# Kernel tuning notes

Measured on AMD Instinct MI355X. Metric: run time of the kernel, lower is better.

## Reference

```python
import jax, jax.numpy as jnp
import numpy as np

B, N, C = 4, 2048, 1024
H, D = 16, 64  # num_heads, head_dim; C = H*D
R = 16         # lora rank
SCALE = D ** -0.5


def setup_inputs() -> dict:
    key = jax.random.key(0)
    ks = jax.random.split(key, 6)
    return {
        "query": jax.random.normal(ks[0], (B, N, C), dtype=jnp.float32),
        "mask": jax.random.normal(ks[1], (B, 1, N, N), dtype=jnp.float32),
        "W_qkv": jax.random.normal(ks[2], (C, 3 * C), dtype=jnp.float32) * (C ** -0.5),
        "magnitude": jnp.ones((1, H, 1, 1), dtype=jnp.float32),
        "W_loraA": jax.random.normal(ks[3], (C, R), dtype=jnp.float32) * (C ** -0.5),
        "W_loraB": jax.random.normal(ks[4], (R, C), dtype=jnp.float32) * (R ** -0.5),
        "W_proj": jax.random.normal(ks[5], (C, C), dtype=jnp.float32) * (C ** -0.5),
    }


def reference(query, mask, W_qkv, magnitude, W_loraA, W_loraB, W_proj):
    # qkv projection: [B,N,3C] -> [3,B,H,N,D]
    qkv = (query @ W_qkv).reshape(B, N, 3, H, D).transpose(2, 0, 3, 1, 4)
    q, k, v = qkv[0], qkv[1], qkv[2]
    # LoRA/DoRA delta fused into q before attention
    delta = (query @ W_loraA) @ W_loraB                     # [B,N,C]
    delta = delta.reshape(B, N, H, D).transpose(0, 2, 1, 3)  # [B,H,N,D]
    q = q + magnitude * delta
    # attention
    attn = jnp.einsum('bhnd,bhmd->bhnm', q, k) * SCALE + mask
    attn = jax.nn.softmax(attn, axis=-1)
    out = jnp.einsum('bhnm,bhmd->bhnd', attn, v)            # [B,H,N,D]
    out = out.transpose(0, 2, 1, 3).reshape(B, N, C)
    return out @ W_proj
```

## Files before the change

kernel.cpp:

```cpp
#include <hip/hip_runtime.h>
#include <hip/hip_bf16.h>

#define Bd 4
#define Nd 2048
#define Cd 1024
#define Hd 16
#define Dd 64
#define Rd 16
#define KAUG 1056
#define SCALEf 0.125f
#define PIT 72

using short8 = __attribute__((ext_vector_type(8))) short;
using f32x4  = __attribute__((ext_vector_type(4))) float;

static __device__ __forceinline__ ushort f2bf(float f) {
    __hip_bfloat16 h = __float2bfloat16(f);
    return *reinterpret_cast<ushort*>(&h);
}

#define GLOAD_LDS16(g, l) __builtin_amdgcn_global_load_lds( \
    (const __attribute__((address_space(1))) void*)(g),      \
    (__attribute__((address_space(3))) void*)(l), 16, 0, 0)

__global__ __launch_bounds__(256) void pack_a_kernel(
    const float* __restrict__ query, ushort* __restrict__ Aaug)
{
    const int row = blockIdx.x;
    const int t = threadIdx.x;
    const float4 v = *(const float4*)&query[(size_t)row * Cd + t * 4];
    ushort4 u;
    u.x = f2bf(v.x); u.y = f2bf(v.y); u.z = f2bf(v.z); u.w = f2bf(v.w);
    *(ushort4*)&Aaug[(size_t)row * KAUG + t * 4] = u;
}

__global__ __launch_bounds__(256) void pack_wat_kernel(
    const float* __restrict__ WA, ushort* __restrict__ WAT)
{
    const int idx = blockIdx.x * 256 + threadIdx.x;
    const int c = idx >> 4, r = idx & 15;
    WAT[r * 1024 + c] = f2bf(WA[idx]);
}

__global__ __launch_bounds__(64) void lora_mfma_kernel(
    const ushort* __restrict__ Aro, const ushort* __restrict__ WAT,
    ushort* __restrict__ Awr)
{
    const int lane = threadIdx.x;
    const int quad = lane >> 4, lc = lane & 15;
    const int row0 = blockIdx.x * 16;
    f32x4 acc = {0.f, 0.f, 0.f, 0.f};
    #pragma unroll 4
    for (int k0 = 0; k0 < 1024; k0 += 32) {
        const short8 a = *(const short8*)&Aro[(size_t)(row0 + lc) * KAUG + k0 + quad * 8];
        const short8 b = *(const short8*)&WAT[lc * 1024 + k0 + quad * 8];
        acc = __builtin_amdgcn_mfma_f32_16x16x32_bf16(a, b, acc, 0, 0, 0);
    }
    #pragma unroll
    for (int ri = 0; ri < 4; ++ri) {
        const size_t row = row0 + quad * 4 + ri;
        Awr[row * KAUG + 1024 + lc] = f2bf(acc[ri]);
        Awr[row * KAUG + 1040 + lc] = 0;
    }
}

__global__ __launch_bounds__(256) void pack_bqkv_kernel(
    const float* __restrict__ Wqkv, const float* __restrict__ WloraB,
    const float* __restrict__ magnitude, ushort* __restrict__ BT)
{
    __shared__ float tile[32][33];
    const int k0 = blockIdx.x * 32, n0 = blockIdx.y * 32;
    const int tx = threadIdx.x & 31, ty = threadIdx.x >> 5;
    #pragma unroll
    for (int i = 0; i < 4; ++i) {
        const int k = k0 + ty + i * 8;
        const int n = n0 + tx;
        float v;
        if (k < 1024)                      v = Wqkv[(size_t)k * 3072 + n];
        else if (k < 1040 && n < 1024)     v = magnitude[n >> 6] * WloraB[(k - 1024) * Cd + n];
        else                               v = 0.f;
        tile[ty + i * 8][tx] = v;
    }
    __syncthreads();
    #pragma unroll
    for (int i = 0; i < 4; ++i) {
        const int n = n0 + ty + i * 8;
        const int k = k0 + tx;
        BT[(size_t)n * KAUG + k] = f2bf(tile[tx][ty + i * 8]);
    }
}

__global__ __launch_bounds__(256) void pack_bproj_kernel(
    const float* __restrict__ Wp, ushort* __restrict__ BT)
{
    __shared__ float tile[32][33];
    const int k0 = blockIdx.x * 32, n0 = blockIdx.y * 32;
    const int tx = threadIdx.x & 31, ty = threadIdx.x >> 5;
    #pragma unroll
    for (int i = 0; i < 4; ++i)
        tile[ty + i * 8][tx] = Wp[(size_t)(k0 + ty + i * 8) * Cd + n0 + tx];
    __syncthreads();
    #pragma unroll
    for (int i = 0; i < 4; ++i)
        BT[(size_t)(n0 + ty + i * 8) * Cd + k0 + tx] = f2bf(tile[tx][ty + i * 8]);
}

template <int KD, int MODE>
__global__ __launch_bounds__(256) void mfma_gemm_kernel(
    const ushort* __restrict__ Ag, const ushort* __restrict__ Bg,
    ushort* __restrict__ qb, ushort* __restrict__ kb, ushort* __restrict__ vb,
    float* __restrict__ outf)
{
    __shared__ ushort As[128 * 32];
    __shared__ ushort Bs[128 * 32];
    const int t = threadIdx.x;
    const int w = t >> 6, lane = t & 63, quad = lane >> 4, lc = lane & 15;
    const int wm = w >> 1, wn = w & 1;
    const int m0 = blockIdx.y * 128, n0 = blockIdx.x * 128;

    f32x4 acc[4][4] = {};

    const int lin0 = t, lin1 = t + 256;
    const int rowT0 = lin0 >> 2, kc0 = (lin0 & 3) * 8;
    const int rowT1 = lin1 >> 2, kc1 = (lin1 & 3) * 8;

    for (int k0 = 0; k0 < KD; k0 += 32) {
        GLOAD_LDS16(&Ag[(size_t)(m0 + rowT0) * KD + k0 + kc0], &As[lin0 * 8]);
        GLOAD_LDS16(&Ag[(size_t)(m0 + rowT1) * KD + k0 + kc1], &As[lin1 * 8]);
        GLOAD_LDS16(&Bg[(size_t)(n0 + rowT0) * KD + k0 + kc0], &Bs[lin0 * 8]);
        GLOAD_LDS16(&Bg[(size_t)(n0 + rowT1) * KD + k0 + kc1], &Bs[lin1 * 8]);
        __syncthreads();
        short8 a[4], b[4];
        #pragma unroll
        for (int i = 0; i < 4; ++i)
            a[i] = *(const short8*)&As[(wm * 64 + i * 16 + lc) * 32 + quad * 8];
        #pragma unroll
        for (int j = 0; j < 4; ++j)
            b[j] = *(const short8*)&Bs[(wn * 64 + j * 16 + lc) * 32 + quad * 8];
        #pragma unroll
        for (int i = 0; i < 4; ++i)
            #pragma unroll
            for (int j = 0; j < 4; ++j)
                acc[i][j] = __builtin_amdgcn_mfma_f32_16x16x32_bf16(a[i], b[j], acc[i][j], 0, 0, 0);
        __syncthreads();
    }

    if (MODE == 0) {
        const int sec = n0 >> 10;
        ushort* dst = sec == 0 ? qb : (sec == 1 ? kb : vb);
        #pragma unroll
        for (int i = 0; i < 4; ++i)
            #pragma unroll
            for (int j = 0; j < 4; ++j) {
                const int gcol = (n0 & 1023) + wn * 64 + j * 16 + lc;
                const int h = gcol >> 6, d = gcol & 63;
                #pragma unroll
                for (int r = 0; r < 4; ++r) {
                    const int grow = m0 + wm * 64 + i * 16 + quad * 4 + r;
                    const int b_ = grow >> 11, n_ = grow & 2047;
                    dst[(((size_t)(b_ * Hd) + h) * Nd + n_) * Dd + d] = f2bf(acc[i][j][r]);
                }
            }
    } else {
        #pragma unroll
        for (int i = 0; i < 4; ++i)
            #pragma unroll
            for (int j = 0; j < 4; ++j) {
                const int gcol = n0 + wn * 64 + j * 16 + lc;
                #pragma unroll
                for (int r = 0; r < 4; ++r) {
                    const int grow = m0 + wm * 64 + i * 16 + quad * 4 + r;
                    outf[(size_t)grow * Cd + gcol] = acc[i][j][r];
                }
            }
    }
}

__global__ __launch_bounds__(256) void attn_mfma_kernel(
    const ushort* __restrict__ qbuf, const ushort* __restrict__ kbuf,
    const ushort* __restrict__ vbuf, const float* __restrict__ mask,
    ushort* __restrict__ attn_out)
{
    __shared__ short Qs[64 * PIT];
    __shared__ short Ks[64 * PIT];
    __shared__ short Vts[64 * PIT];
    __shared__ short Ps[64 * PIT];

    const int t = threadIdx.x;
    const int w = t >> 6, lane = t & 63;
    const int quad = lane >> 4, lc = lane & 15;
    const int bh = blockIdx.y, b = bh >> 4, h = bh & 15;
    const int n0 = blockIdx.x * 64;

    const short* qg = (const short*)qbuf + (size_t)bh * Nd * Dd;
    const short* kg = (const short*)kbuf + (size_t)bh * Nd * Dd;
    const short* vg = (const short*)vbuf + (size_t)bh * Nd * Dd;
    const float* mbase = mask + ((size_t)b * Nd + n0) * Nd;

    {
        const int row = t >> 2, dblk = (t & 3) * 16;
        *(int4*)&Qs[row * PIT + dblk]     = *(const int4*)&qg[(n0 + row) * Dd + dblk];
        *(int4*)&Qs[row * PIT + dblk + 8] = *(const int4*)&qg[(n0 + row) * Dd + dblk + 8];
    }

    float rs[4] = {0.f, 0.f, 0.f, 0.f};
    f32x4 o[4];
    #pragma unroll
    for (int dt = 0; dt < 4; ++dt) o[dt] = (f32x4){0.f, 0.f, 0.f, 0.f};

    const int rowg = w * 16 + quad * 4;

    for (int m0 = 0; m0 < Nd; m0 += 64) {
        {
            const int row = t >> 2, dblk = (t & 3) * 16;
            *(int4*)&Ks[row * PIT + dblk]     = *(const int4*)&kg[(m0 + row) * Dd + dblk];
            *(int4*)&Ks[row * PIT + dblk + 8] = *(const int4*)&kg[(m0 + row) * Dd + dblk + 8];
        }
        {
            const int kv0 = (t >> 3) * 2;
            const int dg = t & 7, d0 = dg * 8;
            ushort u0[8], u1[8];
            *(int4*)u0 = *(const int4*)&vg[(m0 + kv0) * Dd + d0];
            *(int4*)u1 = *(const int4*)&vg[(m0 + kv0 + 1) * Dd + d0];
            const int blk = ((kv0 >> 3) ^ dg) & 7;
            #pragma unroll
            for (int i = 0; i < 8; ++i) {
                *(uint*)&Vts[(d0 + i) * PIT + blk * 8 + (kv0 & 7)] =
                    (uint)u0[i] | ((uint)u1[i] << 16);
            }
        }
        float mk[4][4];
        #pragma unroll
        for (int r = 0; r < 4; ++r)
            #pragma unroll
            for (int nt = 0; nt < 4; ++nt)
                mk[r][nt] = mbase[(size_t)(rowg + r) * Nd + m0 + nt * 16 + lc];
        __syncthreads();

        f32x4 s[4];
        #pragma unroll
        for (int nt = 0; nt < 4; ++nt) s[nt] = (f32x4){0.f, 0.f, 0.f, 0.f};
        #pragma unroll
        for (int ks = 0; ks < 2; ++ks) {
            const short8 a = *(const short8*)&Qs[(w * 16 + lc) * PIT + ks * 32 + quad * 8];
            #pragma unroll
            for (int nt = 0; nt < 4; ++nt) {
                const short8 bb = *(const short8*)&Ks[(nt * 16 + lc) * PIT + ks * 32 + quad * 8];
                s[nt] = __builtin_amdgcn_mfma_f32_16x16x32_bf16(a, bb, s[nt], 0, 0, 0);
            }
        }
        #pragma unroll
        for (int nt = 0; nt < 4; ++nt) {
            const int cbx = ((nt * 2 + (lc >> 3)) ^ quad) * 8 + (lc & 7);
            #pragma unroll
            for (int r = 0; r < 4; ++r) {
                const float p = __expf(fmaf(s[nt][r], SCALEf, mk[r][nt]));
                rs[r] += p;
                Ps[(rowg + r) * PIT + cbx] = (short)f2bf(p);
            }
        }
        #pragma unroll
        for (int ks = 0; ks < 2; ++ks) {
            const int pblk = (((ks * 4 + quad) ^ ((lc >> 2) & 3)) & 7) * 8;
            const short8 a = *(const short8*)&Ps[(w * 16 + lc) * PIT + pblk];
            #pragma unroll
            for (int dt = 0; dt < 4; ++dt) {
                const int d = dt * 16 + lc;
                const int blk = (ks * 4 + quad) ^ ((d >> 3) & 7);
                const short8 bb = *(const short8*)&Vts[d * PIT + blk * 8];
                o[dt] = __builtin_amdgcn_mfma_f32_16x16x32_bf16(a, bb, o[dt], 0, 0, 0);
            }
        }
        __syncthreads();
    }

    #pragma unroll
    for (int r = 0; r < 4; ++r) {
        float v = rs[r];
        v += __shfl_xor(v, 1);
        v += __shfl_xor(v, 2);
        v += __shfl_xor(v, 4);
        v += __shfl_xor(v, 8);
        const float inv = 1.f / v;
        const size_t rowo = ((size_t)(b * Nd + n0 + rowg + r)) * Cd + h * Dd;
        #pragma unroll
        for (int dt = 0; dt < 4; ++dt)
            attn_out[rowo + dt * 16 + lc] = f2bf(o[dt][r] * inv);
    }
}

extern "C" void kernel_launch(void* const* d_in, const int* in_sizes, int n_in,
                              void* d_out, int out_size, void* d_ws, size_t ws_size,
                              hipStream_t stream) {
    const float* query     = (const float*)d_in[0];
    const float* mask      = (const float*)d_in[1];
    const float* Wqkv      = (const float*)d_in[2];
    const float* magnitude = (const float*)d_in[3];
    const float* WloraA    = (const float*)d_in[4];
    const float* WloraB    = (const float*)d_in[5];
    const float* Wproj     = (const float*)d_in[6];
    float* out = (float*)d_out;

    const size_t SZ = (size_t)Bd * Hd * Nd * Dd;
    char* p = (char*)d_ws;
    ushort* qbuf = (ushort*)p;           p += SZ * 2;
    ushort* kbuf = (ushort*)p;           p += SZ * 2;
    ushort* vbuf = (ushort*)p;           p += SZ * 2;
    ushort* aout = (ushort*)p;           p += SZ * 2;
    ushort* Aaug = (ushort*)p;           p += (size_t)8192 * KAUG * 2;
    ushort* BT   = (ushort*)p;           p += (size_t)3072 * KAUG * 2;
    ushort* WpT  = (ushort*)p;           p += (size_t)1024 * 1024 * 2;
    ushort* WAT  = (ushort*)p;           p += (size_t)16 * 1024 * 2;

    pack_a_kernel<<<dim3(Bd * Nd), 256, 0, stream>>>(query, Aaug);
    pack_wat_kernel<<<dim3(64), 256, 0, stream>>>(WloraA, WAT);
    pack_bqkv_kernel<<<dim3(KAUG / 32, 3072 / 32), 256, 0, stream>>>(
        Wqkv, WloraB, magnitude, BT);
    pack_bproj_kernel<<<dim3(32, 32), 256, 0, stream>>>(Wproj, WpT);
    lora_mfma_kernel<<<dim3(512), 64, 0, stream>>>(Aaug, WAT, Aaug);
    mfma_gemm_kernel<KAUG, 0><<<dim3(24, 64), 256, 0, stream>>>(
        Aaug, BT, qbuf, kbuf, vbuf, nullptr);
    attn_mfma_kernel<<<dim3(Nd / 64, Bd * Hd), 256, 0, stream>>>(
        qbuf, kbuf, vbuf, mask, aout);
    mfma_gemm_kernel<1024, 1><<<dim3(8, 64), 256, 0, stream>>>(
        aout, WpT, nullptr, nullptr, nullptr, out);
}
```

Before: 411.4 us.

## Compute transposed S tile so mask loads and P stores vectorize

```diff
diff --git a/kernel.cpp b/kernel.cpp
--- a/kernel.cpp
+++ b/kernel.cpp
@@ -195,7 +195,7 @@
     const short* qg = (const short*)qbuf + (size_t)bh * Nd * Dd;
     const short* kg = (const short*)kbuf + (size_t)bh * Nd * Dd;
     const short* vg = (const short*)vbuf + (size_t)bh * Nd * Dd;
-    const float* mbase = mask + ((size_t)b * Nd + n0) * Nd;
+    const float* mrow = mask + ((size_t)b * Nd + n0 + w * 16 + lc) * Nd;
 
     {
         const int row = t >> 2, dblk = (t & 3) * 16;
@@ -203,12 +203,12 @@
         *(int4*)&Qs[row * PIT + dblk + 8] = *(const int4*)&qg[(n0 + row) * Dd + dblk + 8];
     }
 
-    float rs[4] = {0.f, 0.f, 0.f, 0.f};
+    float rsum = 0.f;
     f32x4 o[4];
     #pragma unroll
     for (int dt = 0; dt < 4; ++dt) o[dt] = (f32x4){0.f, 0.f, 0.f, 0.f};
 
-    const int rowg = w * 16 + quad * 4;
+    const int qrow = (w * 16 + lc) * PIT;
 
     for (int m0 = 0; m0 < Nd; m0 += 64) {
         {
@@ -229,12 +229,13 @@
                     (uint)u0[i] | ((uint)u1[i] << 16);
             }
         }
-        float mk[4][4];
-        #pragma unroll
-        for (int r = 0; r < 4; ++r)
+        float4 mk4[4];
+        {
+            const float* mp = mrow + m0 + quad * 4;
             #pragma unroll
             for (int nt = 0; nt < 4; ++nt)
-                mk[r][nt] = mbase[(size_t)(rowg + r) * Nd + m0 + nt * 16 + lc];
+                mk4[nt] = *(const float4*)&mp[nt * 16];
+        }
         __syncthreads();
 
         f32x4 s[4];
@@ -242,27 +243,29 @@
         for (int nt = 0; nt < 4; ++nt) s[nt] = (f32x4){0.f, 0.f, 0.f, 0.f};
         #pragma unroll
         for (int ks = 0; ks < 2; ++ks) {
-            const short8 a = *(const short8*)&Qs[(w * 16 + lc) * PIT + ks * 32 + quad * 8];
+            const short8 qv = *(const short8*)&Qs[qrow + ks * 32 + quad * 8];
             #pragma unroll
             for (int nt = 0; nt < 4; ++nt) {
-                const short8 bb = *(const short8*)&Ks[(nt * 16 + lc) * PIT + ks * 32 + quad * 8];
-                s[nt] = __builtin_amdgcn_mfma_f32_16x16x32_bf16(a, bb, s[nt], 0, 0, 0);
+                const short8 kv = *(const short8*)&Ks[(nt * 16 + lc) * PIT + ks * 32 + quad * 8];
+                s[nt] = __builtin_amdgcn_mfma_f32_16x16x32_bf16(kv, qv, s[nt], 0, 0, 0);
             }
         }
         #pragma unroll
         for (int nt = 0; nt < 4; ++nt) {
-            const int cbx = ((nt * 2 + (lc >> 3)) ^ quad) * 8 + (lc & 7);
-            #pragma unroll
-            for (int r = 0; r < 4; ++r) {
-                const float p = __expf(fmaf(s[nt][r], SCALEf, mk[r][nt]));
-                rs[r] += p;
-                Ps[(rowg + r) * PIT + cbx] = (short)f2bf(p);
-            }
+            const float p0 = __expf(fmaf(s[nt][0], SCALEf, mk4[nt].x));
+            const float p1 = __expf(fmaf(s[nt][1], SCALEf, mk4[nt].y));
+            const float p2 = __expf(fmaf(s[nt][2], SCALEf, mk4[nt].z));
+            const float p3 = __expf(fmaf(s[nt][3], SCALEf, mk4[nt].w));
+            rsum += (p0 + p1) + (p2 + p3);
+            uint lo, hi;
+            asm("v_cvt_pk_bf16_f32 %0, %1, %2" : "=v"(lo) : "v"(p0), "v"(p1));
+            asm("v_cvt_pk_bf16_f32 %0, %1, %2" : "=v"(hi) : "v"(p2), "v"(p3));
+            uint2 pk; pk.x = lo; pk.y = hi;
+            *(uint2*)&Ps[qrow + nt * 16 + quad * 4] = pk;
         }
         #pragma unroll
         for (int ks = 0; ks < 2; ++ks) {
-            const int pblk = (((ks * 4 + quad) ^ ((lc >> 2) & 3)) & 7) * 8;
-            const short8 a = *(const short8*)&Ps[(w * 16 + lc) * PIT + pblk];
+            const short8 a = *(const short8*)&Ps[qrow + ks * 32 + quad * 8];
             #pragma unroll
             for (int dt = 0; dt < 4; ++dt) {
                 const int d = dt * 16 + lc;
@@ -274,15 +277,12 @@
         __syncthreads();
     }
 
+    rsum += __shfl_xor(rsum, 16);
+    rsum += __shfl_xor(rsum, 32);
     #pragma unroll
     for (int r = 0; r < 4; ++r) {
-        float v = rs[r];
-        v += __shfl_xor(v, 1);
-        v += __shfl_xor(v, 2);
-        v += __shfl_xor(v, 4);
-        v += __shfl_xor(v, 8);
-        const float inv = 1.f / v;
-        const size_t rowo = ((size_t)(b * Nd + n0 + rowg + r)) * Cd + h * Dd;
+        const float inv = 1.f / __shfl(rsum, quad * 4 + r);
+        const size_t rowo = ((size_t)(b * Nd + n0 + w * 16 + quad * 4 + r)) * Cd + h * Dd;
         #pragma unroll
         for (int dt = 0; dt < 4; ++dt)
             attn_out[rowo + dt * 16 + lc] = f2bf(o[dt][r] * inv);
```

Result: no change. 416.6 us (+1.3%).

## Double attention query tile to 128 rows per block, keep Q in registers

Applied to the files above, without the earlier changes.

```diff
diff --git a/kernel.cpp b/kernel.cpp
--- a/kernel.cpp
+++ b/kernel.cpp
@@ -181,34 +181,38 @@
     const ushort* __restrict__ vbuf, const float* __restrict__ mask,
     ushort* __restrict__ attn_out)
 {
-    __shared__ short Qs[64 * PIT];
     __shared__ short Ks[64 * PIT];
     __shared__ short Vts[64 * PIT];
-    __shared__ short Ps[64 * PIT];
+    __shared__ short Ps[128 * PIT];
 
     const int t = threadIdx.x;
     const int w = t >> 6, lane = t & 63;
     const int quad = lane >> 4, lc = lane & 15;
     const int bh = blockIdx.y, b = bh >> 4, h = bh & 15;
-    const int n0 = blockIdx.x * 64;
+    const int n0 = blockIdx.x * 128;
 
     const short* qg = (const short*)qbuf + (size_t)bh * Nd * Dd;
     const short* kg = (const short*)kbuf + (size_t)bh * Nd * Dd;
     const short* vg = (const short*)vbuf + (size_t)bh * Nd * Dd;
     const float* mbase = mask + ((size_t)b * Nd + n0) * Nd;
 
-    {
-        const int row = t >> 2, dblk = (t & 3) * 16;
-        *(int4*)&Qs[row * PIT + dblk]     = *(const int4*)&qg[(n0 + row) * Dd + dblk];
-        *(int4*)&Qs[row * PIT + dblk + 8] = *(const int4*)&qg[(n0 + row) * Dd + dblk + 8];
-    }
-
-    float rs[4] = {0.f, 0.f, 0.f, 0.f};
-    f32x4 o[4];
-    #pragma unroll
-    for (int dt = 0; dt < 4; ++dt) o[dt] = (f32x4){0.f, 0.f, 0.f, 0.f};
-
-    const int rowg = w * 16 + quad * 4;
+    short8 qf[2][2];
+    #pragma unroll
+    for (int sub = 0; sub < 2; ++sub)
+        #pragma unroll
+        for (int ks = 0; ks < 2; ++ks)
+            qf[sub][ks] = *(const short8*)
+                &qg[(size_t)(n0 + w * 32 + sub * 16 + lc) * Dd + ks * 32 + quad * 8];
+
+    float rs[2][4];
+    f32x4 o[2][4];
+    #pragma unroll
+    for (int sub = 0; sub < 2; ++sub)
+        #pragma unroll
+        for (int dt = 0; dt < 4; ++dt) {
+            o[sub][dt] = (f32x4){0.f, 0.f, 0.f, 0.f};
+            rs[sub][dt] = 0.f;
+        }
 
     for (int m0 = 0; m0 < Nd; m0 += 64) {
         {
@@ -229,63 +233,84 @@
                     (uint)u0[i] | ((uint)u1[i] << 16);
             }
         }
-        float mk[4][4];
-        #pragma unroll
-        for (int r = 0; r < 4; ++r)
+        float mk[2][4][4];
+        #pragma unroll
+        for (int sub = 0; sub < 2; ++sub)
+            #pragma unroll
+            for (int r = 0; r < 4; ++r)
+                #pragma unroll
+                for (int nt = 0; nt < 4; ++nt)
+                    mk[sub][r][nt] = mbase[(size_t)(w * 32 + sub * 16 + quad * 4 + r) * Nd
+                                           + m0 + nt * 16 + lc];
+        __syncthreads();
+
+        f32x4 s[2][4];
+        #pragma unroll
+        for (int sub = 0; sub < 2; ++sub)
             #pragma unroll
             for (int nt = 0; nt < 4; ++nt)
-                mk[r][nt] = mbase[(size_t)(rowg + r) * Nd + m0 + nt * 16 + lc];
-        __syncthreads();
-
-        f32x4 s[4];
-        #pragma unroll
-        for (int nt = 0; nt < 4; ++nt) s[nt] = (f32x4){0.f, 0.f, 0.f, 0.f};
+                s[sub][nt] = (f32x4){0.f, 0.f, 0.f, 0.f};
+        #pragma unroll
+        for (int ks = 0; ks < 2; ++ks)
+            #pragma unroll
+            for (int nt = 0; nt < 4; ++nt) {
+                const short8 kf = *(const short8*)
+                    &Ks[(nt * 16 + lc) * PIT + ks * 32 + quad * 8];
+                s[0][nt] = __builtin_amdgcn_mfma_f32_16x16x32_bf16(qf[0][ks], kf, s[0][nt], 0, 0, 0);
+                s[1][nt] = __builtin_amdgcn_mfma_f32_16x16x32_bf16(qf[1][ks], kf, s[1][nt], 0, 0, 0);
+            }
+
+        #pragma unroll
+        for (int sub = 0; sub < 2; ++sub) {
+            const int rowg = w * 32 + sub * 16 + quad * 4;
+            #pragma unroll
+            for (int nt = 0; nt < 4; ++nt) {
+                const int cbx = ((nt * 2 + (lc >> 3)) ^ quad) * 8 + (lc & 7);
+                #pragma unroll
+                for (int r = 0; r < 4; ++r) {
+                    const float p = __expf(fmaf(s[sub][nt][r], SCALEf, mk[sub][r][nt]));
+                    rs[sub][r] += p;
+                    Ps[(rowg + r) * PIT + cbx] = (short)f2bf(p);
+                }
+            }
+        }
         #pragma unroll
         for (int ks = 0; ks < 2; ++ks) {
-            const short8 a = *(const short8*)&Qs[(w * 16 + lc) * PIT + ks * 32 + quad * 8];
-            #pragma unroll
-            for (int nt = 0; nt < 4; ++nt) {
-                const short8 bb = *(const short8*)&Ks[(nt * 16 + lc) * PIT + ks * 32 + quad * 8];
-                s[nt] = __builtin_amdgcn_mfma_f32_16x16x32_bf16(a, bb, s[nt], 0, 0, 0);
-            }
-        }
-        #pragma unroll
-        for (int nt = 0; nt < 4; ++nt) {
-            const int cbx = ((nt * 2 + (lc >> 3)) ^ quad) * 8 + (lc & 7);
-            #pragma unroll
-            for (int r = 0; r < 4; ++r) {
-                const float p = __expf(fmaf(s[nt][r], SCALEf, mk[r][nt]));
-                rs[r] += p;
-                Ps[(rowg + r) * PIT + cbx] = (short)f2bf(p);
-            }
-        }
-        #pragma unroll
-        for (int ks = 0; ks < 2; ++ks) {
-            const int pblk = (((ks * 4 + quad) ^ ((lc >> 2) & 3)) & 7) * 8;
-            const short8 a = *(const short8*)&Ps[(w * 16 + lc) * PIT + pblk];
+            short8 bb[4];
             #pragma unroll
             for (int dt = 0; dt < 4; ++dt) {
                 const int d = dt * 16 + lc;
                 const int blk = (ks * 4 + quad) ^ ((d >> 3) & 7);
-                const short8 bb = *(const short8*)&Vts[d * PIT + blk * 8];
-                o[dt] = __builtin_amdgcn_mfma_f32_16x16x32_bf16(a, bb, o[dt], 0, 0, 0);
+                bb[dt] = *(const short8*)&Vts[d * PIT + blk * 8];
+            }
+            const int pblk = (((ks * 4 + quad) ^ ((lc >> 2) & 3)) & 7) * 8;
+            #pragma unroll
+            for (int sub = 0; sub < 2; ++sub) {
+                const short8 a = *(const short8*)&Ps[(w * 32 + sub * 16 + lc) * PIT + pblk];
+                #pragma unroll
+                for (int dt = 0; dt < 4; ++dt)
+                    o[sub][dt] = __builtin_amdgcn_mfma_f32_16x16x32_bf16(a, bb[dt], o[sub][dt], 0, 0, 0);
             }
         }
         __syncthreads();
     }
 
     #pragma unroll
-    for (int r = 0; r < 4; ++r) {
-        float v = rs[r];
-        v += __shfl_xor(v, 1);
-        v += __shfl_xor(v, 2);
-        v += __shfl_xor(v, 4);
-        v += __shfl_xor(v, 8);
-        const float inv = 1.f / v;
-        const size_t rowo = ((size_t)(b * Nd + n0 + rowg + r)) * Cd + h * Dd;
-        #pragma unroll
-        for (int dt = 0; dt < 4; ++dt)
-            attn_out[rowo + dt * 16 + lc] = f2bf(o[dt][r] * inv);
+    for (int sub = 0; sub < 2; ++sub) {
+        const int rowg = w * 32 + sub * 16 + quad * 4;
+        #pragma unroll
+        for (int r = 0; r < 4; ++r) {
+            float v = rs[sub][r];
+            v += __shfl_xor(v, 1);
+            v += __shfl_xor(v, 2);
+            v += __shfl_xor(v, 4);
+            v += __shfl_xor(v, 8);
+            const float inv = 1.f / v;
+            const size_t rowo = ((size_t)(b * Nd + n0 + rowg + r)) * Cd + h * Dd;
+            #pragma unroll
+            for (int dt = 0; dt < 4; ++dt)
+                attn_out[rowo + dt * 16 + lc] = f2bf(o[sub][dt][r] * inv);
+        }
     }
 }
 
@@ -320,7 +345,7 @@
     lora_mfma_kernel<<<dim3(512), 64, 0, stream>>>(Aaug, WAT, Aaug);
     mfma_gemm_kernel<KAUG, 0><<<dim3(24, 64), 256, 0, stream>>>(
         Aaug, BT, qbuf, kbuf, vbuf, nullptr);
-    attn_mfma_kernel<<<dim3(Nd / 64, Bd * Hd), 256, 0, stream>>>(
+    attn_mfma_kernel<<<dim3(Nd / 128, Bd * Hd), 256, 0, stream>>>(
         qbuf, kbuf, vbuf, mask, aout);
     mfma_gemm_kernel<1024, 1><<<dim3(8, 64), 256, 0, stream>>>(
         aout, WpT, nullptr, nullptr, nullptr, out);
```

New measurement: 411.0 us. Within noise of the previous version (-0.1%).
